# Optimization experiments

Hardware: AMD Instinct MI355X
Metric: run time of the kernel (lower is better)

Reference implementation:

```python
import jax, jax.numpy as jnp
import numpy as np

EPS = 1e-5

def gelu(x):
    return jax.nn.gelu(x, approximate=False)  # torch nn.GELU default = exact erf

def bn(x, g, b, m, v):
    # eval-mode BatchNorm1d with running stats; broadcasts over batch axis
    return (x - m) * jax.lax.rsqrt(v + EPS) * g + b

def ln(x, g, b):
    mu = jnp.mean(x, axis=-1, keepdims=True)
    var = jnp.var(x, axis=-1, keepdims=True)
    return (x - mu) * jax.lax.rsqrt(var + EPS) * g + b

def setup_inputs() -> dict:
    B, D, H, E, C = 4096, 512, 1024, 16, 20  # combined dim D = wifi(256)+rfid(256)
    key = jax.random.key(0)
    ks = iter(jax.random.split(key, 40))
    n = lambda shape, s=0.02: jax.random.normal(next(ks), shape, dtype=jnp.float32) * s
    u = lambda shape: jax.random.uniform(next(ks), shape, dtype=jnp.float32, minval=0.5, maxval=1.5)
    inp = {
        'wifi_feat': jax.random.normal(next(ks), (B, 256), dtype=jnp.float32),
        'rfid_feat': jax.random.normal(next(ks), (B, 256), dtype=jnp.float32),
        # gate: Linear(512,1024) -> LayerNorm -> GELU -> Linear(1024,16) -> Softmax
        'gate_w1': n((D, 1024)), 'gate_b1': n((1024,)),
        'gate_ln_g': 1.0 + n((1024,)), 'gate_ln_b': n((1024,)),
        'gate_w2': n((1024, E)), 'gate_b2': n((E,)),
        # experts stacked on leading E axis
        'exp_w1': n((E, D, H)), 'exp_b1': n((E, H)),
        'exp_bn1_g': 1.0 + n((E, H)), 'exp_bn1_b': n((E, H)), 'exp_bn1_m': n((E, H), 0.1), 'exp_bn1_v': u((E, H)),
        'exp_w2': n((E, H, H)), 'exp_b2': n((E, H)),
        'exp_bn2_g': 1.0 + n((E, H)), 'exp_bn2_b': n((E, H)), 'exp_bn2_m': n((E, H), 0.1), 'exp_bn2_v': u((E, H)),
        # final head: Linear(1024,512) -> BN -> GELU -> Linear(512,20)
        'fin_w1': n((H, 512)), 'fin_b1': n((512,)),
        'fin_bn_g': 1.0 + n((512,)), 'fin_bn_b': n((512,)), 'fin_bn_m': n((512,), 0.1), 'fin_bn_v': u((512,)),
        'fin_w2': n((512, C)), 'fin_b2': n((C,)),
    }
    return inp

def reference(wifi_feat, rfid_feat,
              gate_w1, gate_b1, gate_ln_g, gate_ln_b, gate_w2, gate_b2,
              exp_w1, exp_b1, exp_bn1_g, exp_bn1_b, exp_bn1_m, exp_bn1_v,
              exp_w2, exp_b2, exp_bn2_g, exp_bn2_b, exp_bn2_m, exp_bn2_v,
              fin_w1, fin_b1, fin_bn_g, fin_bn_b, fin_bn_m, fin_bn_v,
              fin_w2, fin_b2):
    TOPK = 4
    combined = jnp.concatenate([wifi_feat, rfid_feat], axis=1)  # [B, 512]
    # gate
    g = gelu(ln(combined @ gate_w1 + gate_b1, gate_ln_g, gate_ln_b))
    gate = jax.nn.softmax(g @ gate_w2 + gate_b2, axis=1)  # [B, E]
    topk_gate, topk_idx = jax.lax.top_k(gate, TOPK)  # sorted, matches torch.topk
    topk_gate = jax.nn.softmax(topk_gate, axis=1)  # [B, K]
    # dense all-expert stack (faithful to original torch.stack over experts)
    h = jnp.einsum('bi,eih->ebh', combined, exp_w1) + exp_b1[:, None, :]  # [E,B,H]
    h = gelu(bn(h, exp_bn1_g[:, None, :], exp_bn1_b[:, None, :], exp_bn1_m[:, None, :], exp_bn1_v[:, None, :]))
    h = jnp.einsum('ebh,eho->ebo', h, exp_w2) + exp_b2[:, None, :]
    h = gelu(bn(h, exp_bn2_g[:, None, :], exp_bn2_b[:, None, :], exp_bn2_m[:, None, :], exp_bn2_v[:, None, :]))
    expert_outputs = jnp.transpose(h, (1, 0, 2))  # [B, E, H]
    selected = jnp.take_along_axis(expert_outputs, topk_idx[:, :, None], axis=1)  # [B,K,H]
    fused = jnp.einsum('bkd,bk->bd', selected, topk_gate)  # [B, H]
    # final head
    o = gelu(bn(fused @ fin_w1 + fin_b1, fin_bn_g, fin_bn_b, fin_bn_m, fin_bn_v))
    return o @ fin_w2 + fin_b2  # [B, num_classes]
```

## Files before the change

### kernel.cpp

```cpp
#include <hip/hip_runtime.h>


#define EPSN 1e-5f

typedef __attribute__((ext_vector_type(8))) short v8s;
typedef __attribute__((ext_vector_type(4))) float v4f;

typedef const unsigned int __attribute__((address_space(1)))* gas_u32;
typedef unsigned int __attribute__((address_space(3)))* las_u32;

__device__ __forceinline__ void glds16(const void* g, const void* l) {
    __builtin_amdgcn_global_load_lds((gas_u32)(uintptr_t)g, (las_u32)(uintptr_t)l, 16, 0, 0);
}

__device__ __forceinline__ float gelu_f(float x) {
    return 0.5f * x * (1.0f + erff(x * 0.70710678118654752440f));
}
__device__ __forceinline__ unsigned short f2bf(float x) {
    unsigned int u = __float_as_uint(x);
    u += 0x7fffu + ((u >> 16) & 1u);
    return (unsigned short)(u >> 16);
}
__device__ __forceinline__ float bf2f(unsigned short u) {
    return __uint_as_float(((unsigned int)u) << 16);
}

__global__ __launch_bounds__(256) void concat_kernel(const float4* __restrict__ wifi,
                                                     const float4* __restrict__ rfid,
                                                     float4* __restrict__ comb,
                                                     ushort4* __restrict__ cbf,
                                                     ushort4* __restrict__ cbf3) {
    int gid = blockIdx.x * 256 + threadIdx.x;
    int b = gid >> 7, c = gid & 127;
    float4 v = (c < 64) ? wifi[b * 64 + c] : rfid[b * 64 + (c - 64)];
    comb[gid] = v;
    ushort4 hi, lo;
    hi.x = f2bf(v.x); hi.y = f2bf(v.y); hi.z = f2bf(v.z); hi.w = f2bf(v.w);
    lo.x = f2bf(v.x - bf2f(hi.x));
    lo.y = f2bf(v.y - bf2f(hi.y));
    lo.z = f2bf(v.z - bf2f(hi.z));
    lo.w = f2bf(v.w - bf2f(hi.w));
    cbf[gid] = hi;
    const long r3 = (long)b * 384 + c;
    cbf3[r3]       = hi;
    cbf3[r3 + 128] = lo;
    cbf3[r3 + 256] = hi;
}

__global__ __launch_bounds__(256) void transpose_f2b(const float* __restrict__ in,
                                                     unsigned short* __restrict__ out,
                                                     int K, int N) {
    __shared__ float t[64][65];
    int e = blockIdx.z;
    int n0 = blockIdx.x << 6, k0 = blockIdx.y << 6;
    const float* ie = in + (long)e * K * N;
    unsigned short* oe = out + (long)e * N * K;
    int tid = threadIdx.x;
    int rr = tid >> 4, cc = (tid & 15) << 2;
#pragma unroll
    for (int p = 0; p < 4; ++p) {
        int k = (p << 4) + rr;
        float4 v = *(const float4*)(ie + (long)(k0 + k) * N + n0 + cc);
        t[k][cc + 0] = v.x; t[k][cc + 1] = v.y; t[k][cc + 2] = v.z; t[k][cc + 3] = v.w;
    }
    __syncthreads();
    int n = tid >> 2, kq = (tid & 3) << 4;
    unsigned short u[16];
#pragma unroll
    for (int j = 0; j < 16; ++j) u[j] = f2bf(t[kq + j][n]);
    uint4* dst = (uint4*)(oe + (long)(n0 + n) * K + k0 + kq);
    dst[0] = ((const uint4*)u)[0];
    dst[1] = ((const uint4*)u)[1];
}

__global__ __launch_bounds__(256) void transpose_f2b_hilo(const float* __restrict__ in,
                                                          unsigned short* __restrict__ out,
                                                          int K, int N) {
    __shared__ float t[64][65];
    int n0 = blockIdx.x << 6, k0 = blockIdx.y << 6;
    int tid = threadIdx.x;
    int rr = tid >> 4, cc = (tid & 15) << 2;
#pragma unroll
    for (int p = 0; p < 4; ++p) {
        int k = (p << 4) + rr;
        float4 v = *(const float4*)(in + (long)(k0 + k) * N + n0 + cc);
        t[k][cc + 0] = v.x; t[k][cc + 1] = v.y; t[k][cc + 2] = v.z; t[k][cc + 3] = v.w;
    }
    __syncthreads();
    int n = tid >> 2, kq = (tid & 3) << 4;
    unsigned short uh[16], ul[16];
#pragma unroll
    for (int j = 0; j < 16; ++j) {
        float x = t[kq + j][n];
        unsigned short h = f2bf(x);
        uh[j] = h;
        ul[j] = f2bf(x - bf2f(h));
    }
    unsigned short* dh = out + (long)(n0 + n) * (3 * K) + k0 + kq;
    ((uint4*)dh)[0]           = ((const uint4*)uh)[0];
    ((uint4*)dh)[1]           = ((const uint4*)uh)[1];
    ((uint4*)(dh + K))[0]     = ((const uint4*)uh)[0];
    ((uint4*)(dh + K))[1]     = ((const uint4*)uh)[1];
    ((uint4*)(dh + 2 * K))[0] = ((const uint4*)ul)[0];
    ((uint4*)(dh + 2 * K))[1] = ((const uint4*)ul)[1];
}

__global__ __launch_bounds__(256) void ln_topk_kernel(
    const float* __restrict__ g,
    const float* __restrict__ lng, const float* __restrict__ lnb,
    const float* __restrict__ w2, const float* __restrict__ b2,
    float* __restrict__ wout, int* __restrict__ rows_, int* __restrict__ counts)
{
    __shared__ float gs[1024];
    __shared__ float red[16][17];
    __shared__ float rs[4], rq[4];
    const int b = blockIdx.x;
    const int tid = threadIdx.x;
    const int c = tid << 2;

    float4 v = *(const float4*)(g + (long)b * 1024 + c);
    float s = v.x + v.y + v.z + v.w;
    float q = v.x * v.x + v.y * v.y + v.z * v.z + v.w * v.w;
    for (int off = 32; off > 0; off >>= 1) {
        s += __shfl_down(s, off);
        q += __shfl_down(q, off);
    }
    int wid = tid >> 6;
    if ((tid & 63) == 0) { rs[wid] = s; rq[wid] = q; }
    __syncthreads();
    float S = rs[0] + rs[1] + rs[2] + rs[3];
    float Q = rq[0] + rq[1] + rq[2] + rq[3];
    float mu = S * (1.0f / 1024.0f);
    float var = Q * (1.0f / 1024.0f) - mu * mu;
    float rstd = rsqrtf(var + EPSN);
    gs[c + 0] = gelu_f((v.x - mu) * rstd * lng[c + 0] + lnb[c + 0]);
    gs[c + 1] = gelu_f((v.y - mu) * rstd * lng[c + 1] + lnb[c + 1]);
    gs[c + 2] = gelu_f((v.z - mu) * rstd * lng[c + 2] + lnb[c + 2]);
    gs[c + 3] = gelu_f((v.w - mu) * rstd * lng[c + 3] + lnb[c + 3]);
    __syncthreads();

    const int e = tid & 15, chunk = tid >> 4;
    float p = 0.f;
#pragma unroll 8
    for (int i = 0; i < 64; ++i) {
        int idx = (chunk << 6) + i;
        p = fmaf(gs[idx], w2[(idx << 4) + e], p);
    }
    red[chunk][e] = p;
    __syncthreads();

    if (tid < 64) {
        float logit = -1e30f;
        if (tid < 16) {
            logit = b2[tid];
#pragma unroll
            for (int cc = 0; cc < 16; ++cc) logit += red[cc][tid];
        }
        float m = logit;
#pragma unroll
        for (int mk = 8; mk >= 1; mk >>= 1) m = fmaxf(m, __shfl_xor(m, mk));
        float pe = (tid < 16) ? expf(logit - m) : 0.f;
        float Z = pe;
#pragma unroll
        for (int mk = 8; mk >= 1; mk >>= 1) Z += __shfl_xor(Z, mk);
        float prob = pe / Z;

        float cur = (tid < 16) ? prob : -1.f;
        const int myi = tid & 15;
        float tv0, tv1, tv2, tv3;
        int ti0, ti1, ti2, ti3;
#define ARGMAX16(TV, TI)                                                     \
        {   float vv = cur; int ii = myi;                                    \
            _Pragma("unroll")                                                \
            for (int mk = 8; mk >= 1; mk >>= 1) {                            \
                float ov = __shfl_xor(vv, mk); int oi = __shfl_xor(ii, mk);  \
                if (ov > vv || (ov == vv && oi < ii)) { vv = ov; ii = oi; }  \
            }                                                                \
            TV = vv; TI = ii;                                                \
            if (myi == ii) cur = -1.f;                                       \
        }
        ARGMAX16(tv0, ti0)
        ARGMAX16(tv1, ti1)
        ARGMAX16(tv2, ti2)
        ARGMAX16(tv3, ti3)
#undef ARGMAX16

        float q0 = 1.f;
        float q1 = expf(tv1 - tv0);
        float q2 = expf(tv2 - tv0);
        float q3 = expf(tv3 - tv0);
        float iZ2 = 1.f / (q0 + q1 + q2 + q3);
        if (tid < 4) {
            float wk = (tid == 0) ? q0 : (tid == 1) ? q1 : (tid == 2) ? q2 : q3;
            int   ee = (tid == 0) ? ti0 : (tid == 1) ? ti1 : (tid == 2) ? ti2 : ti3;
            wout[(b << 2) + tid] = wk * iZ2;
            int j = atomicAdd(&counts[ee], 1);
            rows_[(ee << 12) + j] = (b << 2) | tid;
        }
    }
}

#define WL_MAX 272
__global__ __launch_bounds__(256) void build_wl_kernel(const int* __restrict__ counts,
                                                       int* __restrict__ wl) {
    int t = threadIdx.x;
    for (int i = t; i < WL_MAX; i += 256) wl[i] = -1;
    __syncthreads();
    if (t == 0) {
        int idx = 0;
        for (int e = 0; e < 16; ++e) {
            int nc = (counts[e] + 63) >> 6;
            for (int c = 0; c < nc; ++c) wl[idx++] = (e << 16) | c;
        }
    }
}

template<int ASHIFT, bool GATHER, bool OUTBF, bool WL, bool PLAIN = false>
__global__ __launch_bounds__(256) void mfma_gemm(
    const unsigned short* __restrict__ A, int K,
    const unsigned short* __restrict__ Wt, long wstride,
    const float* __restrict__ bias,
    const float* __restrict__ bng, const float* __restrict__ bnb,
    const float* __restrict__ bnm, const float* __restrict__ bnv,
    int pstride,
    void* __restrict__ outv, int ldo,
    const int* __restrict__ rows_, const int* __restrict__ counts,
    const int* __restrict__ wl, int M)
{
    constexpr int TM = 64;
    int e, m0;
    if constexpr (WL) {
        int w = wl[blockIdx.y];
        if (w < 0) return;
        e = w >> 16;
        m0 = (w & 0xffff) << 6;
    } else {
        e = blockIdx.y;
        m0 = blockIdx.z * TM;
    }
    const int n0 = blockIdx.x << 7;
    const int cnt = GATHER ? counts[e] : M;

    constexpr int AB_USH = 64 * 64 + 128 * 64;
    constexpr int OL_STRIDE = 136;
    constexpr int OL_USH = OUTBF ? TM * OL_STRIDE : 0;
    constexpr int SM_USH = (OL_USH > AB_USH) ? OL_USH : AB_USH;
    __shared__ __align__(16) unsigned short smem[SM_USH];
    unsigned short* Als = smem;
    unsigned short* Bls = smem + 64 * 64;
    __shared__ int rid[TM];
    __shared__ int ain[TM];

    const int tid = threadIdx.x;
    if (tid < TM) {
        int i = m0 + tid;
        int pk, ai;
        if (GATHER) {
            if (i < cnt) { pk = rows_[(e << 12) + i]; ai = pk >> ASHIFT; }
            else { pk = -1; ai = 0; }
        } else { pk = i; ai = i; }
        rid[tid] = pk;
        ain[tid] = ai;
    }
    __syncthreads();

    const int wave = tid >> 6, lane = tid & 63;
    const int wm = (wave >> 1) << 5, wn = (wave & 1) << 6;
    const int lrow = lane & 15, kch = lane >> 4;
    const int wb = wave << 9;

    const int srow = tid >> 3, spos = tid & 7;
    const int skc8 = (spos ^ (srow & 7)) << 3;

    const unsigned short* apa = A + (long)ain[srow] * K + skc8;
    const unsigned short* apb = A + (long)ain[32 + srow] * K + skc8;
    const unsigned short* Wte = Wt + (long)e * wstride;
    const unsigned short* bp0 = Wte + (long)(n0 + srow) * K + skc8;
    const unsigned short* bp1 = Wte + (long)(n0 + 32 + srow) * K + skc8;
    const unsigned short* bp2 = Wte + (long)(n0 + 64 + srow) * K + skc8;
    const unsigned short* bp3 = Wte + (long)(n0 + 96 + srow) * K + skc8;

    v4f acc[2][4] = {};

    const int nk = K >> 6;
    for (int it = 0; it < nk; ++it) {
        glds16(apa, Als + wb);
        glds16(apb, Als + 2048 + wb);
        glds16(bp0, Bls + wb);
        glds16(bp1, Bls + 2048 + wb);
        glds16(bp2, Bls + 4096 + wb);
        glds16(bp3, Bls + 6144 + wb);
        apa += 64; apb += 64; bp0 += 64; bp1 += 64; bp2 += 64; bp3 += 64;
        __syncthreads();

#pragma unroll
        for (int s = 0; s < 2; ++s) {
            const int kc = (s << 2) | kch;
            v8s av[2], bv[4];
#pragma unroll
            for (int f = 0; f < 2; ++f) {
                const int row = wm + (f << 4) + lrow;
                av[f] = *(const v8s*)(Als + row * 64 + ((kc ^ (row & 7)) << 3));
            }
#pragma unroll
            for (int f = 0; f < 4; ++f) {
                const int row = wn + (f << 4) + lrow;
                bv[f] = *(const v8s*)(Bls + row * 64 + ((kc ^ (row & 7)) << 3));
            }
#pragma unroll
            for (int fi = 0; fi < 2; ++fi)
#pragma unroll
                for (int fj = 0; fj < 4; ++fj)
                    acc[fi][fj] = __builtin_amdgcn_mfma_f32_16x16x32_bf16(
                        av[fi], bv[fj], acc[fi][fj], 0, 0, 0);
        }
        __syncthreads();
    }

    if constexpr (OUTBF) {
        unsigned short* Ols = smem;
#pragma unroll
        for (int fj = 0; fj < 4; ++fj) {
            const int c = wn + (fj << 4) + lrow;
            const int pc = e * pstride + n0 + c;
            const float bs = bias[pc];
            const float sc = bng[pc] * rsqrtf(bnv[pc] + EPSN);
            const float mn = bnm[pc], bb = bnb[pc];
#pragma unroll
            for (int fi = 0; fi < 2; ++fi) {
#pragma unroll
                for (int r = 0; r < 4; ++r) {
                    const int lr = wm + (fi << 4) + (kch << 2) + r;
                    float x = acc[fi][fj][r] + bs;
                    x = (x - mn) * sc + bb;
                    x = gelu_f(x);
                    Ols[lr * OL_STRIDE + c] = f2bf(x);
                }
            }
        }
        __syncthreads();
        const int rl = tid >> 4;
        const int c8 = (tid & 15) << 3;
#pragma unroll
        for (int p = 0; p < TM / 16; ++p) {
            const int row = (p << 4) + rl;
            const int orow = rid[row];
            if (orow >= 0) {
                uint4 v = *(const uint4*)(Ols + row * OL_STRIDE + c8);
                *(uint4*)((unsigned short*)outv + (long)orow * ldo + n0 + c8) = v;
            }
        }
    } else {
#pragma unroll
        for (int fj = 0; fj < 4; ++fj) {
            const int c = n0 + wn + (fj << 4) + lrow;
            const int pc = e * pstride + c;
            const float bs = bias[pc];
            float sc = 1.f, mn = 0.f, bb = 0.f;
            if constexpr (!PLAIN) {
                sc = bng[pc] * rsqrtf(bnv[pc] + EPSN);
                mn = bnm[pc]; bb = bnb[pc];
            }
#pragma unroll
            for (int fi = 0; fi < 2; ++fi) {
#pragma unroll
                for (int r = 0; r < 4; ++r) {
                    const int lr = wm + (fi << 4) + (kch << 2) + r;
                    const int orow = rid[lr];
                    if (orow < 0) continue;
                    float x = acc[fi][fj][r] + bs;
                    if constexpr (!PLAIN) {
                        x = (x - mn) * sc + bb;
                        x = gelu_f(x);
                    }
                    ((float*)outv)[(long)orow * ldo + c] = x;
                }
            }
        }
    }
}

__global__ __launch_bounds__(256) void combine_bf_kernel(const ushort4* __restrict__ h2b,
                                                         const float* __restrict__ w,
                                                         ushort4* __restrict__ fusedb) {
    int gid = blockIdx.x * 256 + threadIdx.x;
    int b = gid >> 8, c = gid & 255;
    float a0 = 0.f, a1 = 0.f, a2 = 0.f, a3 = 0.f;
#pragma unroll
    for (int k = 0; k < 4; ++k) {
        float wk = w[b * 4 + k];
        ushort4 v = h2b[(long)(b * 4 + k) * 256 + c];
        a0 += wk * bf2f(v.x); a1 += wk * bf2f(v.y);
        a2 += wk * bf2f(v.z); a3 += wk * bf2f(v.w);
    }
    ushort4 o;
    o.x = f2bf(a0); o.y = f2bf(a1); o.z = f2bf(a2); o.w = f2bf(a3);
    fusedb[gid] = o;
}

__global__ __launch_bounds__(256) void fin2_kernel(const float* __restrict__ o,
                                                   const float* __restrict__ w2,
                                                   const float* __restrict__ b2,
                                                   float* __restrict__ out) {
    __shared__ float ws[512 * 20];
    int tid = threadIdx.x;
    for (int i = tid; i < 512 * 20; i += 256) ws[i] = w2[i];
    __syncthreads();
    int r = blockIdx.x * 64 + (tid >> 2);
    int c0 = (tid & 3) * 5;
    float acc[5];
#pragma unroll
    for (int j = 0; j < 5; ++j) acc[j] = b2[c0 + j];
    const float* orow = o + (long)r * 512;
    for (int i = 0; i < 512; ++i) {
        float v = orow[i];
#pragma unroll
        for (int j = 0; j < 5; ++j) acc[j] += v * ws[i * 20 + c0 + j];
    }
#pragma unroll
    for (int j = 0; j < 5; ++j) out[r * 20 + c0 + j] = acc[j];
}

extern "C" void kernel_launch(void* const* d_in, const int* in_sizes, int n_in,
                              void* d_out, int out_size, void* d_ws, size_t ws_size,
                              hipStream_t stream) {
    const float* wifi    = (const float*)d_in[0];
    const float* rfid    = (const float*)d_in[1];
    const float* gate_w1 = (const float*)d_in[2];
    const float* gate_b1 = (const float*)d_in[3];
    const float* gln_g   = (const float*)d_in[4];
    const float* gln_b   = (const float*)d_in[5];
    const float* gate_w2 = (const float*)d_in[6];
    const float* gate_b2 = (const float*)d_in[7];
    const float* exp_w1  = (const float*)d_in[8];
    const float* exp_b1  = (const float*)d_in[9];
    const float* bn1g    = (const float*)d_in[10];
    const float* bn1b    = (const float*)d_in[11];
    const float* bn1m    = (const float*)d_in[12];
    const float* bn1v    = (const float*)d_in[13];
    const float* exp_w2  = (const float*)d_in[14];
    const float* exp_b2  = (const float*)d_in[15];
    const float* bn2g    = (const float*)d_in[16];
    const float* bn2b    = (const float*)d_in[17];
    const float* bn2m    = (const float*)d_in[18];
    const float* bn2v    = (const float*)d_in[19];
    const float* fin_w1  = (const float*)d_in[20];
    const float* fin_b1  = (const float*)d_in[21];
    const float* fbng    = (const float*)d_in[22];
    const float* fbnb    = (const float*)d_in[23];
    const float* fbnm    = (const float*)d_in[24];
    const float* fbnv    = (const float*)d_in[25];
    const float* fin_w2  = (const float*)d_in[26];
    const float* fin_b2  = (const float*)d_in[27];
    float* out = (float*)d_out;

    const size_t MBy = 1u << 20;
    char* W = (char*)d_ws;
    float*          combined = (float*)         (W + 0);
    unsigned short* cbf      = (unsigned short*)(W + 8 * MBy);
    unsigned short* w1t      = (unsigned short*)(W + 12 * MBy);
    unsigned short* fusedb   = (unsigned short*)(W + 12 * MBy);
    float*          obuf     = (float*)         (W + 20 * MBy);
    unsigned short* w2t      = (unsigned short*)(W + 29 * MBy);
    float*          wq       = (float*)         (W + 61 * MBy);
    int*            rows     = (int*)           (W + 61 * MBy + (1 << 16));
    int*            counts   = (int*)           (W + 61 * MBy + (1 << 16) + (1 << 18));
    int*            wl       = (int*)           (W + 61 * MBy + (1 << 16) + (1 << 18) + 256);
    unsigned short* fw1t     = (unsigned short*)(W + 63 * MBy);
    unsigned short* h1bf     = (unsigned short*)(W + 65 * MBy);
    unsigned short* cbf3     = (unsigned short*)(W + 65 * MBy);
    unsigned short* w1t3     = (unsigned short*)(W + 77 * MBy);
    float*          gbuf     = (float*)         (W + 99 * MBy);
    unsigned short* h2b      = (unsigned short*)(W + 99 * MBy);

    hipMemsetAsync(counts, 0, 16 * sizeof(int), stream);

    concat_kernel<<<2048, 256, 0, stream>>>((const float4*)wifi, (const float4*)rfid,
                                            (float4*)combined, (ushort4*)cbf,
                                            (ushort4*)cbf3);

    transpose_f2b<<<dim3(16, 8, 16), 256, 0, stream>>>(exp_w1, w1t, 512, 1024);
    transpose_f2b<<<dim3(16, 16, 16), 256, 0, stream>>>(exp_w2, w2t, 1024, 1024);
    transpose_f2b<<<dim3(8, 16, 1), 256, 0, stream>>>(fin_w1, fw1t, 1024, 512);
    transpose_f2b_hilo<<<dim3(16, 8, 1), 256, 0, stream>>>(gate_w1, w1t3, 512, 1024);

    mfma_gemm<0, false, false, false, true><<<dim3(8, 1, 64), 256, 0, stream>>>(
        cbf3, 1536, w1t3, 0, gate_b1,
        nullptr, nullptr, nullptr, nullptr, 0,
        gbuf, 1024, nullptr, counts, nullptr, 4096);

    ln_topk_kernel<<<4096, 256, 0, stream>>>(gbuf, gln_g, gln_b, gate_w2, gate_b2,
                                             wq, rows, counts);
    build_wl_kernel<<<1, 256, 0, stream>>>(counts, wl);

    mfma_gemm<2, true, true, true><<<dim3(8, WL_MAX, 1), 256, 0, stream>>>(
        cbf, 512, w1t, (long)512 * 1024, exp_b1,
        bn1g, bn1b, bn1m, bn1v, 1024,
        h1bf, 1024, rows, counts, wl, 4096);

    mfma_gemm<0, true, true, true><<<dim3(8, WL_MAX, 1), 256, 0, stream>>>(
        h1bf, 1024, w2t, (long)1024 * 1024, exp_b2,
        bn2g, bn2b, bn2m, bn2v, 1024,
        h2b, 1024, rows, counts, wl, 4096);

    combine_bf_kernel<<<4096, 256, 0, stream>>>((const ushort4*)h2b, wq, (ushort4*)fusedb);

    mfma_gemm<0, false, false, false><<<dim3(4, 1, 64), 256, 0, stream>>>(
        fusedb, 1024, fw1t, 0, fin_b1,
        fbng, fbnb, fbnm, fbnv, 0,
        obuf, 512, nullptr, counts, nullptr, 4096);

    fin2_kernel<<<64, 256, 0, stream>>>(obuf, fin_w2, fin_b2, out);
}
```

Before: 464.4 us.

## Remap GEMM block order for XCD-local weight reuse and use wave-per-row gate kernel

The expert work list is rebuilt as eight per-XCD lists, each expert covering all N tiles for its M chunks. Blocks are indexed so that blockIdx.x mod 8 picks a list, which keeps all blocks touching the same expert weights on one XCD and its L2. The dense GEMM grids are reordered so M varies fastest. The LayerNorm/top-k gate kernel now uses one wave per row with register-held reductions, which drops shared memory and block barriers. The work list grows to 8192 entries, adding many early-exit blocks, and each XCD list is built by a single thread.

```diff
diff --git a/kernel.cpp b/kernel.cpp
--- a/kernel.cpp
+++ b/kernel.cpp
@@ -105,112 +105,135 @@
     ((uint4*)(dh + 2 * K))[1] = ((const uint4*)ul)[1];
 }
 
-__global__ __launch_bounds__(256) void ln_topk_kernel(
+__global__ __launch_bounds__(256) void ln_topk_wave(
     const float* __restrict__ g,
     const float* __restrict__ lng, const float* __restrict__ lnb,
     const float* __restrict__ w2, const float* __restrict__ b2,
     float* __restrict__ wout, int* __restrict__ rows_, int* __restrict__ counts)
 {
-    __shared__ float gs[1024];
-    __shared__ float red[16][17];
-    __shared__ float rs[4], rq[4];
-    const int b = blockIdx.x;
     const int tid = threadIdx.x;
-    const int c = tid << 2;
-
-    float4 v = *(const float4*)(g + (long)b * 1024 + c);
-    float s = v.x + v.y + v.z + v.w;
-    float q = v.x * v.x + v.y * v.y + v.z * v.z + v.w * v.w;
-    for (int off = 32; off > 0; off >>= 1) {
-        s += __shfl_down(s, off);
-        q += __shfl_down(q, off);
-    }
-    int wid = tid >> 6;
-    if ((tid & 63) == 0) { rs[wid] = s; rq[wid] = q; }
-    __syncthreads();
-    float S = rs[0] + rs[1] + rs[2] + rs[3];
-    float Q = rq[0] + rq[1] + rq[2] + rq[3];
-    float mu = S * (1.0f / 1024.0f);
-    float var = Q * (1.0f / 1024.0f) - mu * mu;
-    float rstd = rsqrtf(var + EPSN);
-    gs[c + 0] = gelu_f((v.x - mu) * rstd * lng[c + 0] + lnb[c + 0]);
-    gs[c + 1] = gelu_f((v.y - mu) * rstd * lng[c + 1] + lnb[c + 1]);
-    gs[c + 2] = gelu_f((v.z - mu) * rstd * lng[c + 2] + lnb[c + 2]);
-    gs[c + 3] = gelu_f((v.w - mu) * rstd * lng[c + 3] + lnb[c + 3]);
-    __syncthreads();
-
-    const int e = tid & 15, chunk = tid >> 4;
-    float p = 0.f;
-#pragma unroll 8
-    for (int i = 0; i < 64; ++i) {
-        int idx = (chunk << 6) + i;
-        p = fmaf(gs[idx], w2[(idx << 4) + e], p);
-    }
-    red[chunk][e] = p;
-    __syncthreads();
-
-    if (tid < 64) {
-        float logit = -1e30f;
-        if (tid < 16) {
-            logit = b2[tid];
-#pragma unroll
-            for (int cc = 0; cc < 16; ++cc) logit += red[cc][tid];
+    const int lane = tid & 63;
+    const int b = (blockIdx.x << 2) + (tid >> 6);
+    const float* row = g + (long)b * 1024;
+    const int c0 = lane << 2;
+
+    float4 xv[4];
+    float s = 0.f, q = 0.f;
+#pragma unroll
+    for (int p = 0; p < 4; ++p) {
+        float4 v = *(const float4*)(row + (p << 8) + c0);
+        xv[p] = v;
+        s += v.x + v.y + v.z + v.w;
+        q += v.x * v.x + v.y * v.y + v.z * v.z + v.w * v.w;
+    }
+#pragma unroll
+    for (int mk = 32; mk >= 1; mk >>= 1) {
+        s += __shfl_xor(s, mk);
+        q += __shfl_xor(q, mk);
+    }
+    const float mu = s * (1.0f / 1024.0f);
+    const float var = q * (1.0f / 1024.0f) - mu * mu;
+    const float rstd = rsqrtf(var + EPSN);
+
+#pragma unroll
+    for (int p = 0; p < 4; ++p) {
+        float4 gv = *(const float4*)(lng + (p << 8) + c0);
+        float4 bv = *(const float4*)(lnb + (p << 8) + c0);
+        xv[p].x = gelu_f((xv[p].x - mu) * rstd * gv.x + bv.x);
+        xv[p].y = gelu_f((xv[p].y - mu) * rstd * gv.y + bv.y);
+        xv[p].z = gelu_f((xv[p].z - mu) * rstd * gv.z + bv.z);
+        xv[p].w = gelu_f((xv[p].w - mu) * rstd * gv.w + bv.w);
+    }
+
+    float a[16];
+#pragma unroll
+    for (int i = 0; i < 16; ++i) a[i] = 0.f;
+#pragma unroll
+    for (int p = 0; p < 4; ++p) {
+        const float xs[4] = {xv[p].x, xv[p].y, xv[p].z, xv[p].w};
+#pragma unroll
+        for (int j = 0; j < 4; ++j) {
+            const int c = (p << 8) + c0 + j;
+            const float4 w0 = *(const float4*)(w2 + (c << 4));
+            const float4 w1 = *(const float4*)(w2 + (c << 4) + 4);
+            const float4 wv2 = *(const float4*)(w2 + (c << 4) + 8);
+            const float4 w3 = *(const float4*)(w2 + (c << 4) + 12);
+            const float xc = xs[j];
+            a[0]  = fmaf(xc, w0.x,  a[0]);  a[1]  = fmaf(xc, w0.y,  a[1]);
+            a[2]  = fmaf(xc, w0.z,  a[2]);  a[3]  = fmaf(xc, w0.w,  a[3]);
+            a[4]  = fmaf(xc, w1.x,  a[4]);  a[5]  = fmaf(xc, w1.y,  a[5]);
+            a[6]  = fmaf(xc, w1.z,  a[6]);  a[7]  = fmaf(xc, w1.w,  a[7]);
+            a[8]  = fmaf(xc, wv2.x, a[8]);  a[9]  = fmaf(xc, wv2.y, a[9]);
+            a[10] = fmaf(xc, wv2.z, a[10]); a[11] = fmaf(xc, wv2.w, a[11]);
+            a[12] = fmaf(xc, w3.x,  a[12]); a[13] = fmaf(xc, w3.y,  a[13]);
+            a[14] = fmaf(xc, w3.z,  a[14]); a[15] = fmaf(xc, w3.w,  a[15]);
         }
-        float m = logit;
-#pragma unroll
-        for (int mk = 8; mk >= 1; mk >>= 1) m = fmaxf(m, __shfl_xor(m, mk));
-        float pe = (tid < 16) ? expf(logit - m) : 0.f;
-        float Z = pe;
-#pragma unroll
-        for (int mk = 8; mk >= 1; mk >>= 1) Z += __shfl_xor(Z, mk);
-        float prob = pe / Z;
-
-        float cur = (tid < 16) ? prob : -1.f;
-        const int myi = tid & 15;
-        float tv0, tv1, tv2, tv3;
-        int ti0, ti1, ti2, ti3;
-#define ARGMAX16(TV, TI)                                                     \
-        {   float vv = cur; int ii = myi;                                    \
-            _Pragma("unroll")                                                \
-            for (int mk = 8; mk >= 1; mk >>= 1) {                            \
-                float ov = __shfl_xor(vv, mk); int oi = __shfl_xor(ii, mk);  \
-                if (ov > vv || (ov == vv && oi < ii)) { vv = ov; ii = oi; }  \
-            }                                                                \
-            TV = vv; TI = ii;                                                \
-            if (myi == ii) cur = -1.f;                                       \
-        }
-        ARGMAX16(tv0, ti0)
-        ARGMAX16(tv1, ti1)
-        ARGMAX16(tv2, ti2)
-        ARGMAX16(tv3, ti3)
-#undef ARGMAX16
-
-        float q0 = 1.f;
-        float q1 = expf(tv1 - tv0);
-        float q2 = expf(tv2 - tv0);
-        float q3 = expf(tv3 - tv0);
-        float iZ2 = 1.f / (q0 + q1 + q2 + q3);
-        if (tid < 4) {
-            float wk = (tid == 0) ? q0 : (tid == 1) ? q1 : (tid == 2) ? q2 : q3;
-            int   ee = (tid == 0) ? ti0 : (tid == 1) ? ti1 : (tid == 2) ? ti2 : ti3;
-            wout[(b << 2) + tid] = wk * iZ2;
-            int j = atomicAdd(&counts[ee], 1);
-            rows_[(ee << 12) + j] = (b << 2) | tid;
-        }
-    }
-}
-
-#define WL_MAX 272
+    }
+#pragma unroll
+    for (int mk = 32; mk >= 1; mk >>= 1) {
+#pragma unroll
+        for (int i = 0; i < 16; ++i) a[i] += __shfl_xor(a[i], mk);
+    }
+#pragma unroll
+    for (int i = 0; i < 16; ++i) a[i] += b2[i];
+
+    float m = a[0];
+#pragma unroll
+    for (int i = 1; i < 16; ++i) m = fmaxf(m, a[i]);
+    float Z = 0.f;
+#pragma unroll
+    for (int i = 0; i < 16; ++i) { a[i] = expf(a[i] - m); Z += a[i]; }
+    const float iZ = 1.0f / Z;
+#pragma unroll
+    for (int i = 0; i < 16; ++i) a[i] *= iZ;
+
+    float tv0, tv1, tv2, tv3;
+    int ti0, ti1, ti2, ti3;
+#define PICK(TV, TI)                                                         \
+    {   float bv = a[0]; int bi = 0;                                         \
+        _Pragma("unroll")                                                    \
+        for (int i = 1; i < 16; ++i) {                                       \
+            bool t = a[i] > bv; bv = t ? a[i] : bv; bi = t ? i : bi;         \
+        }                                                                    \
+        TV = bv; TI = bi;                                                    \
+        _Pragma("unroll")                                                    \
+        for (int i = 0; i < 16; ++i) a[i] = (i == bi) ? -1.f : a[i];         \
+    }
+    PICK(tv0, ti0)
+    PICK(tv1, ti1)
+    PICK(tv2, ti2)
+    PICK(tv3, ti3)
+#undef PICK
+
+    const float q1 = expf(tv1 - tv0);
+    const float q2 = expf(tv2 - tv0);
+    const float q3 = expf(tv3 - tv0);
+    const float iZ2 = 1.0f / (1.0f + q1 + q2 + q3);
+    if (lane < 4) {
+        float wk = (lane == 0) ? 1.f : (lane == 1) ? q1 : (lane == 2) ? q2 : q3;
+        int ee   = (lane == 0) ? ti0 : (lane == 1) ? ti1 : (lane == 2) ? ti2 : ti3;
+        wout[(b << 2) + lane] = wk * iZ2;
+        int j = atomicAdd(&counts[ee], 1);
+        rows_[(ee << 12) + j] = (b << 2) | lane;
+    }
+}
+
+#define WLG 1024
 __global__ __launch_bounds__(256) void build_wl_kernel(const int* __restrict__ counts,
                                                        int* __restrict__ wl) {
     int t = threadIdx.x;
-    for (int i = t; i < WL_MAX; i += 256) wl[i] = -1;
+    for (int i = t; i < 8 * WLG; i += 256) wl[i] = -1;
     __syncthreads();
-    if (t == 0) {
+    if (t < 8) {
+        int* wg = wl + (t << 10);
         int idx = 0;
-        for (int e = 0; e < 16; ++e) {
+#pragma unroll
+        for (int half = 0; half < 2; ++half) {
+            int e = t + (half << 3);
             int nc = (counts[e] + 63) >> 6;
-            for (int c = 0; c < nc; ++c) wl[idx++] = (e << 16) | c;
+            for (int mc = 0; mc < nc; ++mc)
+                for (int x = 0; x < 8; ++x)
+                    wg[idx++] = (e << 16) | (mc << 4) | x;
         }
     }
 }
@@ -228,17 +251,18 @@
     const int* __restrict__ wl, int M)
 {
     constexpr int TM = 64;
-    int e, m0;
+    int e, m0, n0;
     if constexpr (WL) {
-        int w = wl[blockIdx.y];
+        int w = wl[((blockIdx.x & 7) << 10) | (blockIdx.x >> 3)];
         if (w < 0) return;
         e = w >> 16;
-        m0 = (w & 0xffff) << 6;
+        m0 = ((w >> 4) & 0xfff) << 6;
+        n0 = (w & 15) << 7;
     } else {
         e = blockIdx.y;
-        m0 = blockIdx.z * TM;
-    }
-    const int n0 = blockIdx.x << 7;
+        m0 = blockIdx.x * TM;
+        n0 = blockIdx.z << 7;
+    }
     const int cnt = GATHER ? counts[e] : M;
 
     constexpr int AB_USH = 64 * 64 + 128 * 64;
@@ -484,28 +508,28 @@
     transpose_f2b<<<dim3(8, 16, 1), 256, 0, stream>>>(fin_w1, fw1t, 1024, 512);
     transpose_f2b_hilo<<<dim3(16, 8, 1), 256, 0, stream>>>(gate_w1, w1t3, 512, 1024);
 
-    mfma_gemm<0, false, false, false, true><<<dim3(8, 1, 64), 256, 0, stream>>>(
+    mfma_gemm<0, false, false, false, true><<<dim3(64, 1, 8), 256, 0, stream>>>(
         cbf3, 1536, w1t3, 0, gate_b1,
         nullptr, nullptr, nullptr, nullptr, 0,
         gbuf, 1024, nullptr, counts, nullptr, 4096);
 
-    ln_topk_kernel<<<4096, 256, 0, stream>>>(gbuf, gln_g, gln_b, gate_w2, gate_b2,
-                                             wq, rows, counts);
+    ln_topk_wave<<<1024, 256, 0, stream>>>(gbuf, gln_g, gln_b, gate_w2, gate_b2,
+                                           wq, rows, counts);
     build_wl_kernel<<<1, 256, 0, stream>>>(counts, wl);
 
-    mfma_gemm<2, true, true, true><<<dim3(8, WL_MAX, 1), 256, 0, stream>>>(
+    mfma_gemm<2, true, true, true><<<dim3(8 * WLG, 1, 1), 256, 0, stream>>>(
         cbf, 512, w1t, (long)512 * 1024, exp_b1,
         bn1g, bn1b, bn1m, bn1v, 1024,
         h1bf, 1024, rows, counts, wl, 4096);
 
-    mfma_gemm<0, true, true, true><<<dim3(8, WL_MAX, 1), 256, 0, stream>>>(
+    mfma_gemm<0, true, true, true><<<dim3(8 * WLG, 1, 1), 256, 0, stream>>>(
         h1bf, 1024, w2t, (long)1024 * 1024, exp_b2,
         bn2g, bn2b, bn2m, bn2v, 1024,
         h2b, 1024, rows, counts, wl, 4096);
 
     combine_bf_kernel<<<4096, 256, 0, stream>>>((const ushort4*)h2b, wq, (ushort4*)fusedb);
 
-    mfma_gemm<0, false, false, false><<<dim3(4, 1, 64), 256, 0, stream>>>(
+    mfma_gemm<0, false, false, false><<<dim3(64, 1, 4), 256, 0, stream>>>(
         fusedb, 1024, fw1t, 0, fin_b1,
         fbng, fbnb, fbnm, fbnv, 0,
         obuf, 512, nullptr, counts, nullptr, 4096);
```

Measured after the change: 492.0 us. 5.9% more time.
